# Performance work log

Measured on AMD Instinct MI355X. Metric: run time of the kernel, lower is better.

Reference implementation:

```python
import jax, jax.numpy as jnp
import numpy as np

E, H, F, LE, LD, K, CD, DIN = 256, 8, 1024, 4, 3, 8, 4, 4
B, S = 16, 512
SIG2 = 1.0 ** 2 + 1e-8   # dr_sigma**2 + 1e-8
EPS = 1e-5               # LayerNorm / BatchNorm eps


def _ln(x, w, b):
    m = x.mean(-1, keepdims=True)
    v = ((x - m) ** 2).mean(-1, keepdims=True)
    return (x - m) / jnp.sqrt(v + EPS) * w + b


def _gelu(x):
    return jax.nn.gelu(x, approximate=False)  # torch nn.GELU default = exact erf


def _mha(xq, xkv, qkv_w, qkv_b, out_w, out_b, bias=None):
    # torch nn.MultiheadAttention (batch_first), additive float attn bias broadcast over heads
    wq, wk, wv = jnp.split(qkv_w, 3, axis=0)
    bq, bk, bv = jnp.split(qkv_b, 3)
    q = xq @ wq.T + bq
    k = xkv @ wk.T + bk
    v = xkv @ wv.T + bv
    Bn, Tq, Tk = q.shape[0], q.shape[1], k.shape[1]
    hd = E // H
    qh = q.reshape(Bn, Tq, H, hd)
    kh = k.reshape(Bn, Tk, H, hd)
    vh = v.reshape(Bn, Tk, H, hd)
    s = jnp.einsum('bqhd,bkhd->bhqk', qh, kh) / jnp.sqrt(jnp.asarray(hd, q.dtype))
    if bias is not None:
        s = s + bias[:, None]  # same bias for every head
    p = jax.nn.softmax(s, axis=-1)
    o = jnp.einsum('bhqk,bkhd->bqhd', p, vh).reshape(Bn, Tq, E)
    return o @ out_w.T + out_b


def _forward(x, mask, parent_idx, in_w, in_b, bn_w, bn_b, dr_gamma,
             e_qkv_w, e_qkv_b, e_out_w, e_out_b, e_l1_w, e_l1_b, e_l2_w, e_l2_b,
             e_n1_w, e_n1_b, e_n2_w, e_n2_b,
             parent_w, parent_b, query_embed, c1_w, c1_b, c2_w, c2_b,
             d_sqkv_w, d_sqkv_b, d_sout_w, d_sout_b,
             d_cqkv_w, d_cqkv_b, d_cout_w, d_cout_b,
             d_l1_w, d_l1_b, d_l2_w, d_l2_b,
             d_n1_w, d_n1_b, d_n2_w, d_n2_b, d_n3_w, d_n3_b,
             child_w, child_b, o1_w, o1_b, o2_w, o2_b):
    x = jnp.nan_to_num(x)
    # input_dim==4 convention: (log_pt, dEta, dPhi, log_E)
    coords = jnp.stack([x[..., 1], x[..., 2]], axis=-1)          # [B,S,2]
    # input_proj: Linear -> BatchNorm1d (eval: mean 0, var 1) -> GELU (dropout=identity in eval)
    h = x @ in_w.T + in_b
    h = (h / jnp.sqrt(1.0 + EPS)) * bn_w + bn_b
    h = _gelu(h)
    # dR Gaussian attention bias: [B,S,S]; mask is all-valid so no -inf fill
    d = coords[:, :, None, :] - coords[:, None, :, :]
    dr2 = d[..., 0] ** 2 + d[..., 1] ** 2
    bias = -(dr_gamma[0] * dr2) / (2.0 * SIG2)
    # dR-biased pre-norm encoder
    for i in range(LE):
        hn = _ln(h, e_n1_w[i], e_n1_b[i])
        h = h + _mha(hn, hn, e_qkv_w[i], e_qkv_b[i], e_out_w[i], e_out_b[i], bias)
        hn = _ln(h, e_n2_w[i], e_n2_b[i])
        h = h + _gelu(hn @ e_l1_w[i].T + e_l1_b[i]) @ e_l2_w[i].T + e_l2_b[i]
    memory = jnp.nan_to_num(h)
    parent_logit = (memory @ parent_w.T + parent_b)[..., 0]       # [B,S]
    # conditional decoder queries
    p = memory[jnp.arange(memory.shape[0]), parent_idx]           # [B,E]
    m = mask.astype(memory.dtype)
    g = (memory * m[..., None]).sum(1) / jnp.maximum(m.sum(1, keepdims=True), 1.0)
    cond = _gelu(jnp.concatenate([p, g], -1) @ c1_w.T + c1_b) @ c2_w.T + c2_b
    t = query_embed[None] + cond[:, None]                         # [B,K,E]
    # pre-norm transformer decoder (self-attn, cross-attn, ff)
    for i in range(LD):
        tn = _ln(t, d_n1_w[i], d_n1_b[i])
        t = t + _mha(tn, tn, d_sqkv_w[i], d_sqkv_b[i], d_sout_w[i], d_sout_b[i])
        tn = _ln(t, d_n2_w[i], d_n2_b[i])
        t = t + _mha(tn, memory, d_cqkv_w[i], d_cqkv_b[i], d_cout_w[i], d_cout_b[i])
        tn = _ln(t, d_n3_w[i], d_n3_b[i])
        t = t + _gelu(tn @ d_l1_w[i].T + d_l1_b[i]) @ d_l2_w[i].T + d_l2_b[i]
    child_feat = t @ child_w.T + child_b                          # [B,K,CD]
    obj_logit = (_gelu(t @ o1_w.T + o1_b) @ o2_w.T + o2_b)[..., 0]  # [B,K]
    return parent_logit, child_feat, obj_logit


def setup_inputs() -> dict:
    key = jax.random.key(0)
    ks = iter(jax.random.split(key, 64))
    def w(shape, scale=0.05):
        return jax.random.normal(next(ks), shape, jnp.float32) * scale
    return {
        'x': jax.random.normal(next(ks), (B, S, DIN), jnp.float32),
        'mask': jnp.ones((B, S), dtype=bool),
        'parent_idx': jax.random.randint(next(ks), (B,), 0, S),
        'in_w': w((E, DIN)), 'in_b': jnp.zeros((E,)),
        'bn_w': jnp.ones((E,)), 'bn_b': jnp.zeros((E,)),
        'dr_gamma': jnp.ones((1,)),
        'e_qkv_w': w((LE, 3 * E, E)), 'e_qkv_b': jnp.zeros((LE, 3 * E)),
        'e_out_w': w((LE, E, E)), 'e_out_b': jnp.zeros((LE, E)),
        'e_l1_w': w((LE, F, E)), 'e_l1_b': jnp.zeros((LE, F)),
        'e_l2_w': w((LE, E, F)), 'e_l2_b': jnp.zeros((LE, E)),
        'e_n1_w': jnp.ones((LE, E)), 'e_n1_b': jnp.zeros((LE, E)),
        'e_n2_w': jnp.ones((LE, E)), 'e_n2_b': jnp.zeros((LE, E)),
        'parent_w': w((1, E)), 'parent_b': jnp.zeros((1,)),
        'query_embed': w((K, E), 0.02),
        'c1_w': w((E, 2 * E)), 'c1_b': jnp.zeros((E,)),
        'c2_w': w((E, E)), 'c2_b': jnp.zeros((E,)),
        'd_sqkv_w': w((LD, 3 * E, E)), 'd_sqkv_b': jnp.zeros((LD, 3 * E)),
        'd_sout_w': w((LD, E, E)), 'd_sout_b': jnp.zeros((LD, E)),
        'd_cqkv_w': w((LD, 3 * E, E)), 'd_cqkv_b': jnp.zeros((LD, 3 * E)),
        'd_cout_w': w((LD, E, E)), 'd_cout_b': jnp.zeros((LD, E)),
        'd_l1_w': w((LD, F, E)), 'd_l1_b': jnp.zeros((LD, F)),
        'd_l2_w': w((LD, E, F)), 'd_l2_b': jnp.zeros((LD, E)),
        'd_n1_w': jnp.ones((LD, E)), 'd_n1_b': jnp.zeros((LD, E)),
        'd_n2_w': jnp.ones((LD, E)), 'd_n2_b': jnp.zeros((LD, E)),
        'd_n3_w': jnp.ones((LD, E)), 'd_n3_b': jnp.zeros((LD, E)),
        'child_w': w((CD, E)), 'child_b': jnp.zeros((CD,)),
        'o1_w': w((E, E)), 'o1_b': jnp.zeros((E,)),
        'o2_w': w((1, E)), 'o2_b': jnp.zeros((1,)),
    }


def reference(x, mask, parent_idx, in_w, in_b, bn_w, bn_b, dr_gamma,
              e_qkv_w, e_qkv_b, e_out_w, e_out_b, e_l1_w, e_l1_b, e_l2_w, e_l2_b,
              e_n1_w, e_n1_b, e_n2_w, e_n2_b,
              parent_w, parent_b, query_embed, c1_w, c1_b, c2_w, c2_b,
              d_sqkv_w, d_sqkv_b, d_sout_w, d_sout_b,
              d_cqkv_w, d_cqkv_b, d_cout_w, d_cout_b,
              d_l1_w, d_l1_b, d_l2_w, d_l2_b,
              d_n1_w, d_n1_b, d_n2_w, d_n2_b, d_n3_w, d_n3_b,
              child_w, child_b, o1_w, o1_b, o2_w, o2_b):
    return _forward(x, mask, parent_idx, in_w, in_b, bn_w, bn_b, dr_gamma,
                    e_qkv_w, e_qkv_b, e_out_w, e_out_b, e_l1_w, e_l1_b, e_l2_w, e_l2_b,
                    e_n1_w, e_n1_b, e_n2_w, e_n2_b,
                    parent_w, parent_b, query_embed, c1_w, c1_b, c2_w, c2_b,
                    d_sqkv_w, d_sqkv_b, d_sout_w, d_sout_b,
                    d_cqkv_w, d_cqkv_b, d_cout_w, d_cout_b,
                    d_l1_w, d_l1_b, d_l2_w, d_l2_b,
                    d_n1_w, d_n1_b, d_n2_w, d_n2_b, d_n3_w, d_n3_b,
                    child_w, child_b, o1_w, o1_b, o2_w, o2_b)
```

## Files before the change

kernel.cpp:

```cpp
#include <hip/hip_runtime.h>
#include <math.h>

#define E 256
#define H 8
#define HD 32
#define FF 1024
#define LE 4
#define LDN 3
#define KQ 8
#define CDIM 4
#define DIN 4
#define BATCH 16
#define SEQ 512

typedef __attribute__((ext_vector_type(8))) short s8b;
typedef __attribute__((ext_vector_type(4))) float f32x4;

__device__ __forceinline__ float gelu_f(float x) {
  return 0.5f * x * (1.f + erff(x * 0.70710678118654752f));
}

__device__ __forceinline__ unsigned short f2b(float f) {
  union { float f; unsigned u; } a;
  a.f = f;
  unsigned r = (a.u + 0x7fffu + ((a.u >> 16) & 1u)) >> 16;
  return (unsigned short)r;
}

__device__ __forceinline__ float b2f(unsigned short u) {
  union { unsigned u; float f; } a;
  a.u = ((unsigned)u) << 16;
  return a.f;
}

__device__ __forceinline__ void gload16(const unsigned short* g, unsigned short* l) {
  __builtin_amdgcn_global_load_lds((const __attribute__((address_space(1))) void*)g,
                                   (__attribute__((address_space(3))) void*)l, 16, 0, 0);
}

template <int GELU, int OMODE>
__global__ __launch_bounds__(256) void mfma_gemm64o_kernel(
    const unsigned short* __restrict__ A, const unsigned short* __restrict__ Wt,
    const float* __restrict__ bias, unsigned short* __restrict__ outb,
    unsigned short* __restrict__ vtb, int N, int K) {
  __shared__ __align__(16) unsigned short As[64 * 32];
  __shared__ __align__(16) unsigned short Bs[128 * 32];
  int tid = threadIdx.x;
  int lane = tid & 63, w = tid >> 6;
  int row0 = blockIdx.y * 64, col0 = blockIdx.x * 128;
  int wr = (w >> 1) * 32, wc = (w & 1) * 64;
  f32x4 acc[2][4] = {};

  int sc = lane & 3;
  int srA = w * 16 + (lane >> 2);
  int gcA = (sc ^ ((srA >> 1) & 3)) * 8;
  const unsigned short* ApA = A + (size_t)(row0 + srA) * K + gcA;
  unsigned short* lA = As + (w * 16) * 32;
  int sr0 = w * 32 + (lane >> 2);
  int sr1 = sr0 + 16;
  int gc0 = (sc ^ ((sr0 >> 1) & 3)) * 8;
  int gc1 = (sc ^ ((sr1 >> 1) & 3)) * 8;
  const unsigned short* Bp0 = Wt + (size_t)(col0 + sr0) * K + gc0;
  const unsigned short* Bp1 = Wt + (size_t)(col0 + sr1) * K + gc1;
  unsigned short* lB0 = Bs + (w * 32) * 32;
  unsigned short* lB1 = Bs + (w * 32 + 16) * 32;

  for (int k0 = 0; k0 < K; k0 += 32) {
    __syncthreads();
    gload16(ApA + k0, lA);
    gload16(Bp0 + k0, lB0);
    gload16(Bp1 + k0, lB1);
    __syncthreads();
    int krow = lane & 15, kq = lane >> 4;
    s8b afr[2], bfr[4];
    #pragma unroll
    for (int mi = 0; mi < 2; ++mi) {
      int r = wr + mi * 16 + krow;
      afr[mi] = *(const s8b*)(As + r * 32 + ((kq ^ ((r >> 1) & 3)) * 8));
    }
    #pragma unroll
    for (int ni = 0; ni < 4; ++ni) {
      int r = wc + ni * 16 + krow;
      bfr[ni] = *(const s8b*)(Bs + r * 32 + ((kq ^ ((r >> 1) & 3)) * 8));
    }
    #pragma unroll
    for (int mi = 0; mi < 2; ++mi)
      #pragma unroll
      for (int ni = 0; ni < 4; ++ni)
        acc[mi][ni] = __builtin_amdgcn_mfma_f32_16x16x32_bf16(afr[mi], bfr[ni], acc[mi][ni], 0, 0, 0);
  }

  int cl = lane & 15, rb = (lane >> 4) * 4;
  #pragma unroll
  for (int ni = 0; ni < 4; ++ni) {
    int col = col0 + wc + ni * 16 + cl;
    float bv = bias[col];
    #pragma unroll
    for (int mi = 0; mi < 2; ++mi) {
      #pragma unroll
      for (int j = 0; j < 4; ++j) {
        int row = row0 + wr + mi * 16 + rb + j;
        float v = acc[mi][ni][j] + bv;
        if (GELU) v = gelu_f(v);
        if (OMODE == 1) {
          outb[(size_t)row * N + col] = f2b(v);
        } else {
          int b = row >> 9, s = row & 511;
          int sect = col >> 8, hh = (col >> 5) & 7, d = col & 31;
          if (sect < 2)
            outb[((((size_t)sect * BATCH + b) * H + hh) * SEQ + s) * HD + d] = f2b(v);
          else
            vtb[(((size_t)b * H + hh) * HD + d) * SEQ + s] = f2b(v);
        }
      }
    }
  }
}

__global__ __launch_bounds__(256) void mfma_gemm32_kernel(
    const unsigned short* __restrict__ A, const unsigned short* __restrict__ Wt,
    const float* __restrict__ bias, const float* __restrict__ resid,
    float* __restrict__ outf, int M, int N, int K) {
  __shared__ __align__(16) unsigned short As[32 * 32];
  __shared__ __align__(16) unsigned short Bs[128 * 32];
  int tid = threadIdx.x;
  int lane = tid & 63, w = tid >> 6;
  int row0 = blockIdx.y * 32, col0 = blockIdx.x * 128;
  int wr = (w & 1) * 16, wc = (w >> 1) * 64;
  f32x4 acc[4] = {};

  int sc = lane & 3;
  int srA = w * 16 + (lane >> 2);
  int gcA = (sc ^ ((srA >> 1) & 3)) * 8;
  const unsigned short* ApA = A + (size_t)(row0 + (srA & 31)) * K + gcA;
  unsigned short* lA = As + ((w & 1) * 16) * 32;
  int sr0 = w * 32 + (lane >> 2);
  int sr1 = sr0 + 16;
  int gc0 = (sc ^ ((sr0 >> 1) & 3)) * 8;
  int gc1 = (sc ^ ((sr1 >> 1) & 3)) * 8;
  const unsigned short* Bp0 = Wt + (size_t)(col0 + sr0) * K + gc0;
  const unsigned short* Bp1 = Wt + (size_t)(col0 + sr1) * K + gc1;
  unsigned short* lB0 = Bs + (w * 32) * 32;
  unsigned short* lB1 = Bs + (w * 32 + 16) * 32;

  for (int k0 = 0; k0 < K; k0 += 32) {
    __syncthreads();
    if (w < 2) gload16(ApA + k0, lA);
    gload16(Bp0 + k0, lB0);
    gload16(Bp1 + k0, lB1);
    __syncthreads();
    int krow = lane & 15, kq = lane >> 4;
    int ra = wr + krow;
    s8b afr = *(const s8b*)(As + ra * 32 + ((kq ^ ((ra >> 1) & 3)) * 8));
    #pragma unroll
    for (int ni = 0; ni < 4; ++ni) {
      int r = wc + ni * 16 + krow;
      s8b bfr = *(const s8b*)(Bs + r * 32 + ((kq ^ ((r >> 1) & 3)) * 8));
      acc[ni] = __builtin_amdgcn_mfma_f32_16x16x32_bf16(afr, bfr, acc[ni], 0, 0, 0);
    }
  }

  int cl = lane & 15, rb = (lane >> 4) * 4;
  #pragma unroll
  for (int ni = 0; ni < 4; ++ni) {
    int col = col0 + wc + ni * 16 + cl;
    float bv = bias[col];
    #pragma unroll
    for (int j = 0; j < 4; ++j) {
      int row = row0 + wr + rb + j;
      outf[(size_t)row * N + col] = acc[ni][j] + bv + resid[(size_t)row * N + col];
    }
  }
}

__global__ __launch_bounds__(256) void mfma_attn_kernel(
    const unsigned short* __restrict__ qkb, const unsigned short* __restrict__ vt,
    const float2* __restrict__ carr, const float* __restrict__ gamma_p,
    unsigned short* __restrict__ out) {
  __shared__ __align__(16) unsigned short P[4][16 * 64];
  int tid = threadIdx.x, lane = tid & 63, w = tid >> 6;
  int qt = blockIdx.x, h = blockIdx.y, b = blockIdx.z;
  int q0 = qt * 64 + w * 16;
  const unsigned short* qh = qkb + (((size_t)b * H + h) * SEQ) * HD;
  const unsigned short* kh = qkb + ((((size_t)BATCH + b) * H + h) * SEQ) * HD;
  const unsigned short* vh = vt + (((size_t)b * H + h) * HD) * SEQ;
  int r16 = lane & 15, q4 = lane >> 4;
  s8b qa = *(const s8b*)(qh + (size_t)(q0 + r16) * HD + q4 * 8);
  float eq[4], pq[4];
  #pragma unroll
  for (int j = 0; j < 4; ++j) {
    float2 c = carr[b * SEQ + q0 + q4 * 4 + j];
    eq[j] = c.x; pq[j] = c.y;
  }
  float gam = gamma_p[0] * 0.49999999500000004f;
  const float scale = 0.17677669529663687f;
  float m[4], lsum[4];
  #pragma unroll
  for (int j = 0; j < 4; ++j) { m[j] = -1e30f; lsum[j] = 0.f; }
  f32x4 o0 = {}, o1 = {};
  const f32x4 zf = {0.f, 0.f, 0.f, 0.f};
  unsigned short* pw = &P[w][0];

  for (int t = 0; t < SEQ / 64; ++t) {
    int k0 = t * 64;
    f32x4 sf[4];
    #pragma unroll
    for (int f = 0; f < 4; ++f) {
      s8b bk = *(const s8b*)(kh + (size_t)(k0 + f * 16 + r16) * HD + q4 * 8);
      sf[f] = __builtin_amdgcn_mfma_f32_16x16x32_bf16(qa, bk, zf, 0, 0, 0);
    }
    float ek[4], pk[4];
    #pragma unroll
    for (int f = 0; f < 4; ++f) {
      float2 c = carr[b * SEQ + k0 + f * 16 + r16];
      ek[f] = c.x; pk[f] = c.y;
    }
    float sc_[4][4];
    float tmax[4] = {-1e30f, -1e30f, -1e30f, -1e30f};
    #pragma unroll
    for (int f = 0; f < 4; ++f)
      #pragma unroll
      for (int j = 0; j < 4; ++j) {
        float de = eq[j] - ek[f], dp = pq[j] - pk[f];
        float v = sf[f][j] * scale - gam * (de * de + dp * dp);
        sc_[f][j] = v;
        tmax[j] = fmaxf(tmax[j], v);
      }
    #pragma unroll
    for (int j = 0; j < 4; ++j) {
      #pragma unroll
      for (int off = 1; off < 16; off <<= 1)
        tmax[j] = fmaxf(tmax[j], __shfl_xor(tmax[j], off));
      float mn = fmaxf(m[j], tmax[j]);
      float al = __expf(m[j] - mn);
      m[j] = mn;
      lsum[j] *= al;
      o0[j] *= al;
      o1[j] *= al;
    }
    __syncthreads();
    #pragma unroll
    for (int f = 0; f < 4; ++f)
      #pragma unroll
      for (int j = 0; j < 4; ++j) {
        float p = __expf(sc_[f][j] - m[j]);
        lsum[j] += p;
        int prow = q4 * 4 + j;
        int c = f * 16 + r16;
        int chunk = (c >> 3) ^ (prow & 7);
        pw[prow * 64 + chunk * 8 + (c & 7)] = f2b(p);
      }
    __syncthreads();
    #pragma unroll
    for (int ks = 0; ks < 2; ++ks) {
      int chunk = (ks * 4 + q4) ^ (r16 & 7);
      s8b pa = *(const s8b*)(pw + r16 * 64 + chunk * 8);
      s8b v0 = *(const s8b*)(vh + (size_t)r16 * SEQ + k0 + ks * 32 + q4 * 8);
      s8b v1 = *(const s8b*)(vh + (size_t)(16 + r16) * SEQ + k0 + ks * 32 + q4 * 8);
      o0 = __builtin_amdgcn_mfma_f32_16x16x32_bf16(pa, v0, o0, 0, 0, 0);
      o1 = __builtin_amdgcn_mfma_f32_16x16x32_bf16(pa, v1, o1, 0, 0, 0);
    }
  }
  #pragma unroll
  for (int j = 0; j < 4; ++j) {
    #pragma unroll
    for (int off = 1; off < 16; off <<= 1)
      lsum[j] += __shfl_xor(lsum[j], off);
    float inv = 1.f / lsum[j];
    size_t rbase = ((size_t)(b * SEQ + q0 + q4 * 4 + j)) * E + h * HD;
    out[rbase + r16] = f2b(o0[j] * inv);
    out[rbase + 16 + r16] = f2b(o1[j] * inv);
  }
}

__global__ void coords_kernel(const float* __restrict__ x, float2* __restrict__ carr) {
  int i = blockIdx.x * 256 + threadIdx.x;
  if (i >= BATCH * SEQ) return;
  carr[i] = make_float2(x[(size_t)i * DIN + 1], x[(size_t)i * DIN + 2]);
}

__global__ void f2b_kernel(const float* __restrict__ in, unsigned short* __restrict__ out, int n4) {
  int i = blockIdx.x * 256 + threadIdx.x;
  if (i >= n4) return;
  float4 v = ((const float4*)in)[i];
  ushort4 o;
  o.x = f2b(v.x); o.y = f2b(v.y); o.z = f2b(v.z); o.w = f2b(v.w);
  ((ushort4*)out)[i] = o;
}

__global__ void cvt_all_kernel(const float* __restrict__ w0, const float* __restrict__ w1,
                               const float* __restrict__ w2, const float* __restrict__ w3,
                               unsigned short* __restrict__ o0, unsigned short* __restrict__ o1,
                               unsigned short* __restrict__ o2, unsigned short* __restrict__ o3) {
  const int n0 = LE * 3 * E * E / 4, n1 = LE * E * E / 4;
  const int n2 = LE * FF * E / 4, n3 = LE * E * FF / 4;
  int j = blockIdx.x * 256 + threadIdx.x;
  const float* src; unsigned short* dst;
  if (j < n0) { src = w0; dst = o0; }
  else if ((j -= n0) < n1) { src = w1; dst = o1; }
  else if ((j -= n1) < n2) { src = w2; dst = o2; }
  else if ((j -= n2) < n3) { src = w3; dst = o3; }
  else return;
  float4 v = ((const float4*)src)[j];
  ushort4 o;
  o.x = f2b(v.x); o.y = f2b(v.y); o.z = f2b(v.z); o.w = f2b(v.w);
  ((ushort4*)dst)[j] = o;
}

__global__ void kvw_remap_kernel(const float* __restrict__ w, const float* __restrict__ b,
                                 unsigned short* __restrict__ wout, float* __restrict__ bout) {
  int i = blockIdx.x * 256 + threadIdx.x;
  if (i < 1536) bout[i] = b[(i >> 9) * 768 + 256 + (i & 511)];
  if (i >= 98304) return;
  int row = i >> 6, cc = i & 63;
  int l = row >> 9, rr = row & 511;
  const float* src = w + ((size_t)l * 768 + 256 + rr) * 256 + cc * 4;
  float4 v = *(const float4*)src;
  ushort4 o;
  o.x = f2b(v.x); o.y = f2b(v.y); o.z = f2b(v.z); o.w = f2b(v.w);
  *(ushort4*)(wout + (size_t)row * 256 + cc * 4) = o;
}

__global__ __launch_bounds__(256) void input_proj_ln_kernel(
    const float* __restrict__ x, const float* __restrict__ in_w, const float* __restrict__ in_b,
    const float* __restrict__ bn_w, const float* __restrict__ bn_b,
    const float* __restrict__ nw, const float* __restrict__ nb,
    float* __restrict__ h, unsigned short* __restrict__ hn) {
  __shared__ float sred[4];
  __shared__ float vred[4];
  int row = blockIdx.x, e = threadIdx.x;
  const float* xr = x + (size_t)row * DIN;
  float v = in_b[e];
  #pragma unroll
  for (int i = 0; i < DIN; ++i) v += xr[i] * in_w[e * DIN + i];
  v = v * (1.0f / sqrtf(1.0f + 1e-5f)) * bn_w[e] + bn_b[e];
  v = gelu_f(v);
  h[(size_t)row * 256 + e] = v;
  int lane = e & 63, w = e >> 6;
  float s = v;
  #pragma unroll
  for (int off = 32; off > 0; off >>= 1) s += __shfl_xor(s, off);
  if (lane == 0) sred[w] = s;
  __syncthreads();
  float mean = (sred[0] + sred[1] + sred[2] + sred[3]) * (1.f / 256);
  float d = v - mean;
  float vr = d * d;
  #pragma unroll
  for (int off = 32; off > 0; off >>= 1) vr += __shfl_xor(vr, off);
  if (lane == 0) vred[w] = vr;
  __syncthreads();
  float inv = rsqrtf((vred[0] + vred[1] + vred[2] + vred[3]) * (1.f / 256) + 1e-5f);
  hn[(size_t)row * 256 + e] = f2b(d * inv * nw[e] + nb[e]);
}

__global__ __launch_bounds__(256) void ln_bf16_kernel(
    const float* __restrict__ in, const float* __restrict__ w,
    const float* __restrict__ b, unsigned short* __restrict__ out) {
  int r = blockIdx.x * 4 + (threadIdx.x >> 6);
  int l = threadIdx.x & 63;
  const float* p = in + (size_t)r * E;
  float v0 = p[l], v1 = p[l + 64], v2 = p[l + 128], v3 = p[l + 192];
  float s = v0 + v1 + v2 + v3;
  for (int off = 32; off > 0; off >>= 1) s += __shfl_xor(s, off);
  float mean = s * (1.f / E);
  float d0 = v0 - mean, d1 = v1 - mean, d2 = v2 - mean, d3 = v3 - mean;
  float var = d0 * d0 + d1 * d1 + d2 * d2 + d3 * d3;
  for (int off = 32; off > 0; off >>= 1) var += __shfl_xor(var, off);
  float inv = rsqrtf(var * (1.f / E) + 1e-5f);
  unsigned short* o = out + (size_t)r * E;
  o[l]       = f2b(d0 * inv * w[l]       + b[l]);
  o[l + 64]  = f2b(d1 * inv * w[l + 64]  + b[l + 64]);
  o[l + 128] = f2b(d2 * inv * w[l + 128] + b[l + 128]);
  o[l + 192] = f2b(d3 * inv * w[l + 192] + b[l + 192]);
}


template <int N, int GELU>
__global__ __launch_bounds__(256) void dec_ln_gemv_kernel(
    const float* __restrict__ t, const float* __restrict__ nw, const float* __restrict__ nb,
    const float* __restrict__ W, const float* __restrict__ bias, float* __restrict__ outg) {
  __shared__ float X[8][256];
  __shared__ float Pp[4][64][9];
  int b = blockIdx.x, by = blockIdx.y, tid = threadIdx.x;
  const float* tg = t + (size_t)b * 2048;
  int w = tid >> 6, l = tid & 63;
  #pragma unroll
  for (int rr = 0; rr < 2; ++rr) {
    int r = w * 2 + rr;
    float v0 = tg[r * 256 + l], v1 = tg[r * 256 + 64 + l];
    float v2 = tg[r * 256 + 128 + l], v3 = tg[r * 256 + 192 + l];
    float s = v0 + v1 + v2 + v3;
    for (int o = 32; o > 0; o >>= 1) s += __shfl_xor(s, o);
    float mean = s * (1.f / 256);
    float d0 = v0 - mean, d1 = v1 - mean, d2 = v2 - mean, d3 = v3 - mean;
    float var = d0 * d0 + d1 * d1 + d2 * d2 + d3 * d3;
    for (int o = 32; o > 0; o >>= 1) var += __shfl_xor(var, o);
    float inv = rsqrtf(var * (1.f / 256) + 1e-5f);
    X[r][l] = d0 * inv * nw[l] + nb[l];
    X[r][l + 64] = d1 * inv * nw[l + 64] + nb[l + 64];
    X[r][l + 128] = d2 * inv * nw[l + 128] + nb[l + 128];
    X[r][l + 192] = d3 * inv * nw[l + 192] + nb[l + 192];
  }
  __syncthreads();
  int j = tid & 63, kq = tid >> 6;
  int col = by * 64 + j;
  const float4* wp = (const float4*)(W + (size_t)col * 256 + kq * 64);
  float acc[8] = {};
  #pragma unroll
  for (int kk = 0; kk < 16; ++kk) {
    float4 wv = wp[kk];
    int base = kq * 64 + kk * 4;
    #pragma unroll
    for (int r = 0; r < 8; ++r) {
      float4 xv = *(const float4*)&X[r][base];
      acc[r] += xv.x * wv.x + xv.y * wv.y + xv.z * wv.z + xv.w * wv.w;
    }
  }
  #pragma unroll
  for (int r = 0; r < 8; ++r) Pp[kq][j][r] = acc[r];
  __syncthreads();
  for (int i = tid; i < 512; i += 256) {
    int r = i & 7, j2 = i >> 3;
    float v = Pp[0][j2][r] + Pp[1][j2][r] + Pp[2][j2][r] + Pp[3][j2][r] + bias[by * 64 + j2];
    if (GELU) v = gelu_f(v);
    outg[((size_t)b * 8 + r) * N + by * 64 + j2] = v;
  }
}

__global__ __launch_bounds__(256) void dec_selfattn_sout_kernel(
    const float* __restrict__ qkvg, const float* __restrict__ W, const float* __restrict__ bias,
    float* __restrict__ t) {
  __shared__ float QK[8][768];
  __shared__ float S[512];
  __shared__ float X[8][256];
  __shared__ float Pp[4][64][9];
  int b = blockIdx.x, by = blockIdx.y, tid = threadIdx.x;
  const float* qg = qkvg + (size_t)b * 8 * 768;
  for (int i = tid; i < 6144; i += 256) ((float*)QK)[i] = qg[i];
  __syncthreads();
  for (int t2 = tid; t2 < 512; t2 += 256) {
    int h = t2 >> 6, q = (t2 >> 3) & 7, k = t2 & 7;
    const float* qp = &QK[q][h * 32];
    const float* kp = &QK[k][256 + h * 32];
    float d = 0.f;
    #pragma unroll
    for (int jj = 0; jj < 32; ++jj) d += qp[jj] * kp[jj];
    S[t2] = d * 0.17677669529663687f;
  }
  __syncthreads();
  if (tid < 64) {
    float* row = &S[tid * 8];
    float m = row[0];
    #pragma unroll
    for (int k = 1; k < 8; ++k) m = fmaxf(m, row[k]);
    float sum = 0.f;
    #pragma unroll
    for (int k = 0; k < 8; ++k) { float e = __expf(row[k] - m); row[k] = e; sum += e; }
    float inv = 1.f / sum;
    #pragma unroll
    for (int k = 0; k < 8; ++k) row[k] *= inv;
  }
  __syncthreads();
  for (int i = tid; i < 2048; i += 256) {
    int q = i >> 8, c = i & 255, h = c >> 5;
    const float* pr = &S[h * 64 + q * 8];
    float acc = 0.f;
    #pragma unroll
    for (int k = 0; k < 8; ++k) acc += pr[k] * QK[k][512 + c];
    X[q][c] = acc;
  }
  __syncthreads();
  int j = tid & 63, kq = tid >> 6;
  int col = by * 64 + j;
  const float4* wp = (const float4*)(W + (size_t)col * 256 + kq * 64);
  float acc[8] = {};
  #pragma unroll
  for (int kk = 0; kk < 16; ++kk) {
    float4 wv = wp[kk];
    int base = kq * 64 + kk * 4;
    #pragma unroll
    for (int r = 0; r < 8; ++r) {
      float4 xv = *(const float4*)&X[r][base];
      acc[r] += xv.x * wv.x + xv.y * wv.y + xv.z * wv.z + xv.w * wv.w;
    }
  }
  #pragma unroll
  for (int r = 0; r < 8; ++r) Pp[kq][j][r] = acc[r];
  __syncthreads();
  for (int i = tid; i < 512; i += 256) {
    int r = i & 7, j2 = i >> 3;
    float v = Pp[0][j2][r] + Pp[1][j2][r] + Pp[2][j2][r] + Pp[3][j2][r] + bias[by * 64 + j2];
    t[((size_t)b * 8 + r) * 256 + by * 64 + j2] += v;
  }
}

__global__ __launch_bounds__(256) void dec_gemv_resid_kernel(
    const float* __restrict__ Xg, const float* __restrict__ W, const float* __restrict__ bias,
    float* __restrict__ t) {
  __shared__ float X[8][256];
  __shared__ float Pp[4][64][9];
  int b = blockIdx.x, by = blockIdx.y, tid = threadIdx.x;
  const float* xg = Xg + (size_t)b * 2048;
  for (int i = tid; i < 2048; i += 256) ((float*)X)[i] = xg[i];
  __syncthreads();
  int j = tid & 63, kq = tid >> 6;
  int col = by * 64 + j;
  const float4* wp = (const float4*)(W + (size_t)col * 256 + kq * 64);
  float acc[8] = {};
  #pragma unroll
  for (int kk = 0; kk < 16; ++kk) {
    float4 wv = wp[kk];
    int base = kq * 64 + kk * 4;
    #pragma unroll
    for (int r = 0; r < 8; ++r) {
      float4 xv = *(const float4*)&X[r][base];
      acc[r] += xv.x * wv.x + xv.y * wv.y + xv.z * wv.z + xv.w * wv.w;
    }
  }
  #pragma unroll
  for (int r = 0; r < 8; ++r) Pp[kq][j][r] = acc[r];
  __syncthreads();
  for (int i = tid; i < 512; i += 256) {
    int r = i & 7, j2 = i >> 3;
    float v = Pp[0][j2][r] + Pp[1][j2][r] + Pp[2][j2][r] + Pp[3][j2][r] + bias[by * 64 + j2];
    t[((size_t)b * 8 + r) * 256 + by * 64 + j2] += v;
  }
}

__global__ __launch_bounds__(256) void dec_ffn2_kernel(
    const float* __restrict__ MIDg, const float* __restrict__ W, const float* __restrict__ bias,
    float* __restrict__ t) {
  __shared__ float X[8][1024];
  __shared__ float Pp[4][64][9];
  int b = blockIdx.x, by = blockIdx.y, tid = threadIdx.x;
  const float* xg = MIDg + (size_t)b * 8192;
  for (int i = tid; i < 8192; i += 256) ((float*)X)[i] = xg[i];
  __syncthreads();
  int j = tid & 63, kq = tid >> 6;
  int col = by * 64 + j;
  const float4* wp = (const float4*)(W + (size_t)col * 1024 + kq * 256);
  float acc[8] = {};
  #pragma unroll 8
  for (int kk = 0; kk < 64; ++kk) {
    float4 wv = wp[kk];
    int base = kq * 256 + kk * 4;
    #pragma unroll
    for (int r = 0; r < 8; ++r) {
      float4 xv = *(const float4*)&X[r][base];
      acc[r] += xv.x * wv.x + xv.y * wv.y + xv.z * wv.z + xv.w * wv.w;
    }
  }
  #pragma unroll
  for (int r = 0; r < 8; ++r) Pp[kq][j][r] = acc[r];
  __syncthreads();
  for (int i = tid; i < 512; i += 256) {
    int r = i & 7, j2 = i >> 3;
    float v = Pp[0][j2][r] + Pp[1][j2][r] + Pp[2][j2][r] + Pp[3][j2][r] + bias[by * 64 + j2];
    t[((size_t)b * 8 + r) * 256 + by * 64 + j2] += v;
  }
}

__global__ __launch_bounds__(256) void cross_attn_ln_kernel(
    const float* __restrict__ t, const float* __restrict__ nw, const float* __restrict__ nb,
    const float* __restrict__ cqw, const float* __restrict__ cqb,
    const unsigned short* __restrict__ KV, int koff, int voff, float* __restrict__ out) {
  __shared__ float X[256];
  __shared__ float sv[512];
  __shared__ float red[256];
  __shared__ float qv[32];
  __shared__ float pvred[8][32];
  __shared__ float sred[4], vred[4];
  int tid = threadIdx.x;
  int bid = blockIdx.x;
  int q = bid % KQ;
  int h = (bid / KQ) % H;
  int b = bid / (KQ * H);
  {
    float v = t[((size_t)(b * KQ + q)) * 256 + tid];
    int lane = tid & 63, w = tid >> 6;
    float s = v;
    #pragma unroll
    for (int off = 32; off > 0; off >>= 1) s += __shfl_xor(s, off);
    if (lane == 0) sred[w] = s;
    __syncthreads();
    float mean = (sred[0] + sred[1] + sred[2] + sred[3]) * (1.f / 256);
    float d = v - mean;
    float vr = d * d;
    #pragma unroll
    for (int off = 32; off > 0; off >>= 1) vr += __shfl_xor(vr, off);
    if (lane == 0) vred[w] = vr;
    __syncthreads();
    float inv = rsqrtf((vred[0] + vred[1] + vred[2] + vred[3]) * (1.f / 256) + 1e-5f);
    X[tid] = d * inv * nw[tid] + nb[tid];
  }
  __syncthreads();
  {
    int dd = tid >> 3, part = tid & 7;
    int col = h * HD + dd;
    const float4* wp = (const float4*)(cqw + (size_t)col * 256 + part * 32);
    float acc = 0.f;
    #pragma unroll
    for (int kk = 0; kk < 8; ++kk) {
      float4 wv = wp[kk];
      float4 xv = *(const float4*)&X[part * 32 + kk * 4];
      acc += xv.x * wv.x + xv.y * wv.y + xv.z * wv.z + xv.w * wv.w;
    }
    red[tid] = acc;
  }
  __syncthreads();
  if (tid < 32) {
    float acc = 0.f;
    #pragma unroll
    for (int p = 0; p < 8; ++p) acc += red[tid * 8 + p];
    qv[tid] = acc + cqb[h * HD + tid];
  }
  __syncthreads();
  const float scale = 0.17677669529663687f;
  for (int k = tid; k < SEQ; k += 256) {
    const unsigned short* kp = KV + ((size_t)(b * SEQ + k)) * 1536 + koff + h * HD;
    float d = 0.f;
    #pragma unroll
    for (int j4 = 0; j4 < 4; ++j4) {
      s8b kv8 = *(const s8b*)(kp + j4 * 8);
      #pragma unroll
      for (int j = 0; j < 8; ++j)
        d += qv[j4 * 8 + j] * b2f((unsigned short)kv8[j]);
    }
    sv[k] = d * scale;
  }
  __syncthreads();
  float m = -1e30f;
  for (int k = tid; k < SEQ; k += 256) m = fmaxf(m, sv[k]);
  red[tid] = m; __syncthreads();
  for (int s = 128; s > 0; s >>= 1) {
    if (tid < s) red[tid] = fmaxf(red[tid], red[tid + s]);
    __syncthreads();
  }
  m = red[0]; __syncthreads();
  float lsum = 0.f;
  for (int k = tid; k < SEQ; k += 256) { float e = __expf(sv[k] - m); sv[k] = e; lsum += e; }
  red[tid] = lsum; __syncthreads();
  for (int s = 128; s > 0; s >>= 1) {
    if (tid < s) red[tid] += red[tid + s];
    __syncthreads();
  }
  float denom = red[0];
  int d = tid & 31, g = tid >> 5;
  float acc = 0.f;
  for (int k = g; k < SEQ; k += 8)
    acc += sv[k] * b2f(KV[((size_t)(b * SEQ + k)) * 1536 + voff + h * HD + d]);
  pvred[g][d] = acc;
  __syncthreads();
  if (tid < 32) {
    float r = 0.f;
    #pragma unroll
    for (int gg = 0; gg < 8; ++gg) r += pvred[gg][tid];
    out[((size_t)(b * KQ + q)) * E + h * HD + tid] = r / denom;
  }
}

__global__ __launch_bounds__(256) void pool_gather_kernel(
    const float* __restrict__ mem, const int* __restrict__ pidx, float* __restrict__ pg) {
  __shared__ float red[8][32];
  int b = blockIdx.x, cy = blockIdx.y, tid = threadIdx.x;
  int c = cy * 32 + (tid & 31), g = tid >> 5;
  float s = 0.f;
  for (int r = g; r < SEQ; r += 8)
    s += mem[((size_t)b * SEQ + r) * E + c];
  red[g][tid & 31] = s;
  __syncthreads();
  if (tid < 32) {
    float t = 0.f;
    #pragma unroll
    for (int g2 = 0; g2 < 8; ++g2) t += red[g2][tid];
    pg[(size_t)b * 512 + 256 + cy * 32 + tid] = t * (1.f / SEQ);
    pg[(size_t)b * 512 + cy * 32 + tid] = mem[((size_t)b * SEQ + pidx[b]) * E + cy * 32 + tid];
  }
}

__global__ void cond_kernel(const float* __restrict__ pg, const float* __restrict__ c1w,
                            const float* __restrict__ c1b, const float* __restrict__ c2w,
                            const float* __restrict__ c2b, const float* __restrict__ qe,
                            float* __restrict__ t) {
  __shared__ float PG[512];
  __shared__ float C1[256];
  int b = blockIdx.x, c = threadIdx.x;
  PG[c] = pg[(size_t)b * 512 + c];
  PG[c + 256] = pg[(size_t)b * 512 + 256 + c];
  __syncthreads();
  const float4* wp = (const float4*)(c1w + (size_t)c * 512);
  float acc = c1b[c];
  #pragma unroll 8
  for (int kk = 0; kk < 128; ++kk) {
    float4 wv = wp[kk];
    int base = kk * 4;
    acc += PG[base] * wv.x + PG[base + 1] * wv.y + PG[base + 2] * wv.z + PG[base + 3] * wv.w;
  }
  C1[c] = gelu_f(acc);
  __syncthreads();
  const float4* wp2 = (const float4*)(c2w + (size_t)c * 256);
  float acc2 = c2b[c];
  #pragma unroll 8
  for (int kk = 0; kk < 64; ++kk) {
    float4 wv = wp2[kk];
    int base = kk * 4;
    acc2 += C1[base] * wv.x + C1[base + 1] * wv.y + C1[base + 2] * wv.z + C1[base + 3] * wv.w;
  }
  #pragma unroll
  for (int k = 0; k < KQ; ++k)
    t[((size_t)b * KQ + k) * E + c] = qe[k * E + c] + acc2;
}

__global__ void head_kernel(const float* __restrict__ t,
                            const float* __restrict__ childw, const float* __restrict__ childb,
                            const float* __restrict__ o1w, const float* __restrict__ o1b,
                            const float* __restrict__ o2w, const float* __restrict__ o2b,
                            float* __restrict__ out_child, float* __restrict__ out_obj) {
  __shared__ float tr[256];
  __shared__ float red[256];
  int r = blockIdx.x, c = threadIdx.x;
  tr[c] = t[(size_t)r * E + c];
  __syncthreads();
  const float4* wp = (const float4*)(o1w + (size_t)c * 256);
  float acc = o1b[c];
  #pragma unroll 8
  for (int kk = 0; kk < 64; ++kk) {
    float4 wv = wp[kk];
    int base = kk * 4;
    acc += tr[base] * wv.x + tr[base + 1] * wv.y + tr[base + 2] * wv.z + tr[base + 3] * wv.w;
  }
  red[c] = gelu_f(acc) * o2w[c];
  __syncthreads();
  for (int s = 128; s > 0; s >>= 1) {
    if (c < s) red[c] += red[c + s];
    __syncthreads();
  }
  if (c == 0) out_obj[r] = red[0] + o2b[0];
  __syncthreads();
  #pragma unroll
  for (int j = 0; j < CDIM; ++j) {
    red[c] = tr[c] * childw[j * E + c];
    __syncthreads();
    for (int s = 128; s > 0; s >>= 1) {
      if (c < s) red[c] += red[c + s];
      __syncthreads();
    }
    if (c == 0) out_child[r * CDIM + j] = red[0] + childb[j];
    __syncthreads();
  }
}

__global__ void rowdot_kernel(const float* __restrict__ A, const float* __restrict__ w,
                              const float* __restrict__ bias, float* __restrict__ out) {
  int r = blockIdx.x, l = threadIdx.x;
  const float* p = A + (size_t)r * E;
  float s = p[l] * w[l] + p[l + 64] * w[l + 64] + p[l + 128] * w[l + 128] + p[l + 192] * w[l + 192];
  for (int off = 32; off > 0; off >>= 1) s += __shfl_xor(s, off);
  if (l == 0) out[r] = s + bias[0];
}

extern "C" void kernel_launch(void* const* d_in, const int* in_sizes, int n_in,
                              void* d_out, int out_size, void* d_ws, size_t ws_size,
                              hipStream_t stream) {
  const float* x          = (const float*)d_in[0];
  const int*   parent_idx = (const int*)d_in[2];
  const float* in_w  = (const float*)d_in[3];
  const float* in_b  = (const float*)d_in[4];
  const float* bn_w  = (const float*)d_in[5];
  const float* bn_b  = (const float*)d_in[6];
  const float* dr_gamma = (const float*)d_in[7];
  const float* e_qkv_w = (const float*)d_in[8];
  const float* e_qkv_b = (const float*)d_in[9];
  const float* e_out_w = (const float*)d_in[10];
  const float* e_out_b = (const float*)d_in[11];
  const float* e_l1_w = (const float*)d_in[12];
  const float* e_l1_b = (const float*)d_in[13];
  const float* e_l2_w = (const float*)d_in[14];
  const float* e_l2_b = (const float*)d_in[15];
  const float* e_n1_w = (const float*)d_in[16];
  const float* e_n1_b = (const float*)d_in[17];
  const float* e_n2_w = (const float*)d_in[18];
  const float* e_n2_b = (const float*)d_in[19];
  const float* parent_w = (const float*)d_in[20];
  const float* parent_b = (const float*)d_in[21];
  const float* query_embed = (const float*)d_in[22];
  const float* c1_w = (const float*)d_in[23];
  const float* c1_b = (const float*)d_in[24];
  const float* c2_w = (const float*)d_in[25];
  const float* c2_b = (const float*)d_in[26];
  const float* d_sqkv_w = (const float*)d_in[27];
  const float* d_sqkv_b = (const float*)d_in[28];
  const float* d_sout_w = (const float*)d_in[29];
  const float* d_sout_b = (const float*)d_in[30];
  const float* d_cqkv_w = (const float*)d_in[31];
  const float* d_cqkv_b = (const float*)d_in[32];
  const float* d_cout_w = (const float*)d_in[33];
  const float* d_cout_b = (const float*)d_in[34];
  const float* d_l1_w = (const float*)d_in[35];
  const float* d_l1_b = (const float*)d_in[36];
  const float* d_l2_w = (const float*)d_in[37];
  const float* d_l2_b = (const float*)d_in[38];
  const float* d_n1_w = (const float*)d_in[39];
  const float* d_n1_b = (const float*)d_in[40];
  const float* d_n2_w = (const float*)d_in[41];
  const float* d_n2_b = (const float*)d_in[42];
  const float* d_n3_w = (const float*)d_in[43];
  const float* d_n3_b = (const float*)d_in[44];
  const float* child_w = (const float*)d_in[45];
  const float* child_b = (const float*)d_in[46];
  const float* o1_w = (const float*)d_in[47];
  const float* o1_b = (const float*)d_in[48];
  const float* o2_w = (const float*)d_in[49];
  const float* o2_b = (const float*)d_in[50];

  float* out = (float*)d_out;
  const int ROWS = BATCH * SEQ;
  const int TROWS = BATCH * KQ;

  float* ws = (float*)d_ws;
  float* h         = ws;
  float* attnout_d = h + (size_t)ROWS * E;
  float* pg        = attnout_d + (size_t)TROWS * E;
  float* tbuf      = pg + BATCH * 2 * E;
  float* qkv_t     = tbuf + (size_t)TROWS * E;
  float* dmid      = qkv_t + (size_t)TROWS * 3 * E;
  float* kvb3      = dmid + (size_t)TROWS * FF;
  unsigned short* kv_bf   = (unsigned short*)(kvb3 + 1536);
  unsigned short* hn_bf   = kv_bf + (size_t)ROWS * 1536;
  unsigned short* attn_bf = hn_bf + (size_t)ROWS * E;
  unsigned short* mid_bf  = attn_bf + (size_t)ROWS * E;
  unsigned short* eqkv_bf = mid_bf + (size_t)ROWS * FF;
  unsigned short* eout_bf = eqkv_bf + (size_t)LE * 3 * E * E;
  unsigned short* el1_bf  = eout_bf + (size_t)LE * E * E;
  unsigned short* el2_bf  = el1_bf + (size_t)LE * FF * E;
  unsigned short* kvw_bf  = el2_bf + (size_t)LE * E * FF;
  float2* carr = (float2*)(kvw_bf + (size_t)1536 * 256);
  unsigned short* qkb = mid_bf;
  unsigned short* vtb = mid_bf + (size_t)2 * ROWS * E;

  {
    const int total_quads = (LE * 3 * E * E + LE * E * E + LE * FF * E + LE * E * FF) / 4;
    cvt_all_kernel<<<(total_quads + 255) / 256, 256, 0, stream>>>(
        e_qkv_w, e_out_w, e_l1_w, e_l2_w, eqkv_bf, eout_bf, el1_bf, el2_bf);
  }
  kvw_remap_kernel<<<384, 256, 0, stream>>>(d_cqkv_w, d_cqkv_b, kvw_bf, kvb3);
  coords_kernel<<<(BATCH * SEQ + 255) / 256, 256, 0, stream>>>(x, carr);

  input_proj_ln_kernel<<<ROWS, 256, 0, stream>>>(x, in_w, in_b, bn_w, bn_b,
                                                 e_n1_w, e_n1_b, h, hn_bf);

  for (int i = 0; i < LE; ++i) {
    const float* qb = e_qkv_b + (size_t)i * 3 * E;
    const float* ob = e_out_b + (size_t)i * E;
    const float* l1b = e_l1_b + (size_t)i * FF;
    const float* l2b = e_l2_b + (size_t)i * E;
    if (i > 0)
      ln_bf16_kernel<<<ROWS / 4, 256, 0, stream>>>(h, e_n1_w + i * E, e_n1_b + i * E, hn_bf);
    mfma_gemm64o_kernel<0, 2><<<dim3(6, 128), 256, 0, stream>>>(
        hn_bf, eqkv_bf + (size_t)i * 3 * E * E, qb, qkb, vtb, 3 * E, E);
    mfma_attn_kernel<<<dim3(SEQ / 64, H, BATCH), 256, 0, stream>>>(qkb, vtb, carr, dr_gamma, attn_bf);
    mfma_gemm32_kernel<<<dim3(2, 256), 256, 0, stream>>>(
        attn_bf, eout_bf + (size_t)i * E * E, ob, h, h, ROWS, E, E);
    ln_bf16_kernel<<<ROWS / 4, 256, 0, stream>>>(h, e_n2_w + i * E, e_n2_b + i * E, hn_bf);
    mfma_gemm64o_kernel<1, 1><<<dim3(8, 128), 256, 0, stream>>>(
        hn_bf, el1_bf + (size_t)i * FF * E, l1b, mid_bf, nullptr, FF, E);
    mfma_gemm32_kernel<<<dim3(2, 256), 256, 0, stream>>>(
        mid_bf, el2_bf + (size_t)i * E * FF, l2b, h, h, ROWS, E, FF);
  }

  rowdot_kernel<<<ROWS, 64, 0, stream>>>(h, parent_w, parent_b, out);

  pool_gather_kernel<<<dim3(BATCH, 8), 256, 0, stream>>>(h, parent_idx, pg);
  cond_kernel<<<BATCH, 256, 0, stream>>>(pg, c1_w, c1_b, c2_w, c2_b, query_embed, tbuf);

  f2b_kernel<<<(ROWS * E / 4 + 255) / 256, 256, 0, stream>>>(h, hn_bf, ROWS * E / 4);
  mfma_gemm64o_kernel<0, 1><<<dim3(12, 128), 256, 0, stream>>>(
      hn_bf, kvw_bf, kvb3, kv_bf, nullptr, 3 * E * 2, E);

  for (int i = 0; i < LDN; ++i) {
    dec_ln_gemv_kernel<768, 0><<<dim3(BATCH, 12), 256, 0, stream>>>(
        tbuf, d_n1_w + i * E, d_n1_b + i * E,
        d_sqkv_w + (size_t)i * 3 * E * E, d_sqkv_b + (size_t)i * 3 * E, qkv_t);
    dec_selfattn_sout_kernel<<<dim3(BATCH, 4), 256, 0, stream>>>(
        qkv_t, d_sout_w + (size_t)i * E * E, d_sout_b + (size_t)i * E, tbuf);
    cross_attn_ln_kernel<<<BATCH * H * KQ, 256, 0, stream>>>(
        tbuf, d_n2_w + i * E, d_n2_b + i * E,
        d_cqkv_w + (size_t)i * 3 * E * E, d_cqkv_b + (size_t)i * 3 * E,
        kv_bf, i * 512, i * 512 + 256, attnout_d);
    dec_gemv_resid_kernel<<<dim3(BATCH, 4), 256, 0, stream>>>(
        attnout_d, d_cout_w + (size_t)i * E * E, d_cout_b + (size_t)i * E, tbuf);
    dec_ln_gemv_kernel<1024, 1><<<dim3(BATCH, 16), 256, 0, stream>>>(
        tbuf, d_n3_w + i * E, d_n3_b + i * E,
        d_l1_w + (size_t)i * FF * E, d_l1_b + (size_t)i * FF, dmid);
    dec_ffn2_kernel<<<dim3(BATCH, 4), 256, 0, stream>>>(
        dmid, d_l2_w + (size_t)i * E * FF, d_l2_b + (size_t)i * E, tbuf);
  }

  head_kernel<<<TROWS, 256, 0, stream>>>(tbuf, child_w, child_b, o1_w, o1_b, o2_w, o2_b,
                                         out + ROWS, out + ROWS + TROWS * CDIM);
}
```

Baseline: 748.6 us.

## Fuse LayerNorm and bf16 cast into residual GEMM epilogue with full-row tiles

The residual-add GEMM now gives each block 32 full rows of all 256 output columns, so the epilogue can compute the row LayerNorm across the block and write the bf16 normalized activations directly. This removes the separate ln_bf16 kernels and the final f2b cast kernel. Each layer saves launches and a full read of the fp32 hidden state. In exchange there are half as many blocks (256 instead of 512) and more accumulator registers per thread, which may lower occupancy for the K=1024 GEMM.

```diff
diff --git a/kernel.cpp b/kernel.cpp
--- a/kernel.cpp
+++ b/kernel.cpp
@@ -117,58 +117,115 @@
   }
 }
 
-__global__ __launch_bounds__(256) void mfma_gemm32_kernel(
+template <int LNMODE>
+__global__ __launch_bounds__(256) void mfma_gemm32n256_ln_kernel(
     const unsigned short* __restrict__ A, const unsigned short* __restrict__ Wt,
-    const float* __restrict__ bias, const float* __restrict__ resid,
-    float* __restrict__ outf, int M, int N, int K) {
+    const float* __restrict__ bias, float* __restrict__ h,
+    const float* __restrict__ nw, const float* __restrict__ nb,
+    unsigned short* __restrict__ hn, int K) {
   __shared__ __align__(16) unsigned short As[32 * 32];
-  __shared__ __align__(16) unsigned short Bs[128 * 32];
+  __shared__ __align__(16) unsigned short Bs[256 * 32];
+  __shared__ float psum[2][32];
+  __shared__ float pvar[2][32];
   int tid = threadIdx.x;
   int lane = tid & 63, w = tid >> 6;
-  int row0 = blockIdx.y * 32, col0 = blockIdx.x * 128;
-  int wr = (w & 1) * 16, wc = (w >> 1) * 64;
-  f32x4 acc[4] = {};
+  int row0 = blockIdx.x * 32;
+  int wr = (w & 1) * 16, wc = (w >> 1) * 128;
+  int ch = w >> 1;
+  f32x4 acc[8] = {};
 
   int sc = lane & 3;
   int srA = w * 16 + (lane >> 2);
   int gcA = (sc ^ ((srA >> 1) & 3)) * 8;
   const unsigned short* ApA = A + (size_t)(row0 + (srA & 31)) * K + gcA;
   unsigned short* lA = As + ((w & 1) * 16) * 32;
-  int sr0 = w * 32 + (lane >> 2);
-  int sr1 = sr0 + 16;
-  int gc0 = (sc ^ ((sr0 >> 1) & 3)) * 8;
-  int gc1 = (sc ^ ((sr1 >> 1) & 3)) * 8;
-  const unsigned short* Bp0 = Wt + (size_t)(col0 + sr0) * K + gc0;
-  const unsigned short* Bp1 = Wt + (size_t)(col0 + sr1) * K + gc1;
-  unsigned short* lB0 = Bs + (w * 32) * 32;
-  unsigned short* lB1 = Bs + (w * 32 + 16) * 32;
+  const unsigned short* BpB[4];
+  unsigned short* lB[4];
+  #pragma unroll
+  for (int is = 0; is < 4; ++is) {
+    int srB = w * 64 + is * 16 + (lane >> 2);
+    int gcB = (sc ^ ((srB >> 1) & 3)) * 8;
+    BpB[is] = Wt + (size_t)srB * K + gcB;
+    lB[is] = Bs + (w * 64 + is * 16) * 32;
+  }
 
   for (int k0 = 0; k0 < K; k0 += 32) {
     __syncthreads();
     if (w < 2) gload16(ApA + k0, lA);
-    gload16(Bp0 + k0, lB0);
-    gload16(Bp1 + k0, lB1);
+    #pragma unroll
+    for (int is = 0; is < 4; ++is) gload16(BpB[is] + k0, lB[is]);
     __syncthreads();
     int krow = lane & 15, kq = lane >> 4;
     int ra = wr + krow;
     s8b afr = *(const s8b*)(As + ra * 32 + ((kq ^ ((ra >> 1) & 3)) * 8));
     #pragma unroll
-    for (int ni = 0; ni < 4; ++ni) {
-      int r = wc + ni * 16 + krow;
+    for (int nf = 0; nf < 8; ++nf) {
+      int r = wc + nf * 16 + krow;
       s8b bfr = *(const s8b*)(Bs + r * 32 + ((kq ^ ((r >> 1) & 3)) * 8));
-      acc[ni] = __builtin_amdgcn_mfma_f32_16x16x32_bf16(afr, bfr, acc[ni], 0, 0, 0);
+      acc[nf] = __builtin_amdgcn_mfma_f32_16x16x32_bf16(afr, bfr, acc[nf], 0, 0, 0);
     }
   }
 
   int cl = lane & 15, rb = (lane >> 4) * 4;
   #pragma unroll
-  for (int ni = 0; ni < 4; ++ni) {
-    int col = col0 + wc + ni * 16 + cl;
+  for (int nf = 0; nf < 8; ++nf) {
+    int col = wc + nf * 16 + cl;
     float bv = bias[col];
     #pragma unroll
     for (int j = 0; j < 4; ++j) {
       int row = row0 + wr + rb + j;
-      outf[(size_t)row * N + col] = acc[ni][j] + bv + resid[(size_t)row * N + col];
+      float v = acc[nf][j] + bv + h[(size_t)row * 256 + col];
+      acc[nf][j] = v;
+      h[(size_t)row * 256 + col] = v;
+    }
+  }
+  if (LNMODE == 0) {
+    float mean_[4], inv_[4];
+    #pragma unroll
+    for (int j = 0; j < 4; ++j) {
+      float s = 0.f;
+      #pragma unroll
+      for (int nf = 0; nf < 8; ++nf) s += acc[nf][j];
+      s += __shfl_xor(s, 1); s += __shfl_xor(s, 2);
+      s += __shfl_xor(s, 4); s += __shfl_xor(s, 8);
+      if (cl == 0) psum[ch][wr + rb + j] = s;
+    }
+    __syncthreads();
+    #pragma unroll
+    for (int j = 0; j < 4; ++j)
+      mean_[j] = (psum[0][wr + rb + j] + psum[1][wr + rb + j]) * (1.f / 256);
+    #pragma unroll
+    for (int j = 0; j < 4; ++j) {
+      float vv = 0.f;
+      #pragma unroll
+      for (int nf = 0; nf < 8; ++nf) { float d = acc[nf][j] - mean_[j]; vv += d * d; }
+      vv += __shfl_xor(vv, 1); vv += __shfl_xor(vv, 2);
+      vv += __shfl_xor(vv, 4); vv += __shfl_xor(vv, 8);
+      if (cl == 0) pvar[ch][wr + rb + j] = vv;
+    }
+    __syncthreads();
+    #pragma unroll
+    for (int j = 0; j < 4; ++j)
+      inv_[j] = rsqrtf((pvar[0][wr + rb + j] + pvar[1][wr + rb + j]) * (1.f / 256) + 1e-5f);
+    #pragma unroll
+    for (int nf = 0; nf < 8; ++nf) {
+      int col = wc + nf * 16 + cl;
+      float nwv = nw[col], nbv = nb[col];
+      #pragma unroll
+      for (int j = 0; j < 4; ++j) {
+        int row = row0 + wr + rb + j;
+        hn[(size_t)row * 256 + col] = f2b((acc[nf][j] - mean_[j]) * inv_[j] * nwv + nbv);
+      }
+    }
+  } else {
+    #pragma unroll
+    for (int nf = 0; nf < 8; ++nf) {
+      int col = wc + nf * 16 + cl;
+      #pragma unroll
+      for (int j = 0; j < 4; ++j) {
+        int row = row0 + wr + rb + j;
+        hn[(size_t)row * 256 + col] = f2b(acc[nf][j]);
+      }
     }
   }
 }
@@ -277,15 +334,6 @@
   int i = blockIdx.x * 256 + threadIdx.x;
   if (i >= BATCH * SEQ) return;
   carr[i] = make_float2(x[(size_t)i * DIN + 1], x[(size_t)i * DIN + 2]);
-}
-
-__global__ void f2b_kernel(const float* __restrict__ in, unsigned short* __restrict__ out, int n4) {
-  int i = blockIdx.x * 256 + threadIdx.x;
-  if (i >= n4) return;
-  float4 v = ((const float4*)in)[i];
-  ushort4 o;
-  o.x = f2b(v.x); o.y = f2b(v.y); o.z = f2b(v.z); o.w = f2b(v.w);
-  ((ushort4*)out)[i] = o;
 }
 
 __global__ void cvt_all_kernel(const float* __restrict__ w0, const float* __restrict__ w1,
@@ -351,27 +399,6 @@
   __syncthreads();
   float inv = rsqrtf((vred[0] + vred[1] + vred[2] + vred[3]) * (1.f / 256) + 1e-5f);
   hn[(size_t)row * 256 + e] = f2b(d * inv * nw[e] + nb[e]);
-}
-
-__global__ __launch_bounds__(256) void ln_bf16_kernel(
-    const float* __restrict__ in, const float* __restrict__ w,
-    const float* __restrict__ b, unsigned short* __restrict__ out) {
-  int r = blockIdx.x * 4 + (threadIdx.x >> 6);
-  int l = threadIdx.x & 63;
-  const float* p = in + (size_t)r * E;
-  float v0 = p[l], v1 = p[l + 64], v2 = p[l + 128], v3 = p[l + 192];
-  float s = v0 + v1 + v2 + v3;
-  for (int off = 32; off > 0; off >>= 1) s += __shfl_xor(s, off);
-  float mean = s * (1.f / E);
-  float d0 = v0 - mean, d1 = v1 - mean, d2 = v2 - mean, d3 = v3 - mean;
-  float var = d0 * d0 + d1 * d1 + d2 * d2 + d3 * d3;
-  for (int off = 32; off > 0; off >>= 1) var += __shfl_xor(var, off);
-  float inv = rsqrtf(var * (1.f / E) + 1e-5f);
-  unsigned short* o = out + (size_t)r * E;
-  o[l]       = f2b(d0 * inv * w[l]       + b[l]);
-  o[l + 64]  = f2b(d1 * inv * w[l + 64]  + b[l + 64]);
-  o[l + 128] = f2b(d2 * inv * w[l + 128] + b[l + 128]);
-  o[l + 192] = f2b(d3 * inv * w[l + 192] + b[l + 192]);
 }
 
 
@@ -854,18 +881,22 @@
     const float* ob = e_out_b + (size_t)i * E;
     const float* l1b = e_l1_b + (size_t)i * FF;
     const float* l2b = e_l2_b + (size_t)i * E;
-    if (i > 0)
-      ln_bf16_kernel<<<ROWS / 4, 256, 0, stream>>>(h, e_n1_w + i * E, e_n1_b + i * E, hn_bf);
     mfma_gemm64o_kernel<0, 2><<<dim3(6, 128), 256, 0, stream>>>(
         hn_bf, eqkv_bf + (size_t)i * 3 * E * E, qb, qkb, vtb, 3 * E, E);
     mfma_attn_kernel<<<dim3(SEQ / 64, H, BATCH), 256, 0, stream>>>(qkb, vtb, carr, dr_gamma, attn_bf);
-    mfma_gemm32_kernel<<<dim3(2, 256), 256, 0, stream>>>(
-        attn_bf, eout_bf + (size_t)i * E * E, ob, h, h, ROWS, E, E);
-    ln_bf16_kernel<<<ROWS / 4, 256, 0, stream>>>(h, e_n2_w + i * E, e_n2_b + i * E, hn_bf);
+    mfma_gemm32n256_ln_kernel<0><<<256, 256, 0, stream>>>(
+        attn_bf, eout_bf + (size_t)i * E * E, ob, h,
+        e_n2_w + i * E, e_n2_b + i * E, hn_bf, E);
     mfma_gemm64o_kernel<1, 1><<<dim3(8, 128), 256, 0, stream>>>(
         hn_bf, el1_bf + (size_t)i * FF * E, l1b, mid_bf, nullptr, FF, E);
-    mfma_gemm32_kernel<<<dim3(2, 256), 256, 0, stream>>>(
-        mid_bf, el2_bf + (size_t)i * E * FF, l2b, h, h, ROWS, E, FF);
+    if (i < LE - 1)
+      mfma_gemm32n256_ln_kernel<0><<<256, 256, 0, stream>>>(
+          mid_bf, el2_bf + (size_t)i * E * FF, l2b, h,
+          e_n1_w + (i + 1) * E, e_n1_b + (i + 1) * E, hn_bf, FF);
+    else
+      mfma_gemm32n256_ln_kernel<1><<<256, 256, 0, stream>>>(
+          mid_bf, el2_bf + (size_t)i * E * FF, l2b, h,
+          nullptr, nullptr, hn_bf, FF);
   }
 
   rowdot_kernel<<<ROWS, 64, 0, stream>>>(h, parent_w, parent_b, out);
@@ -873,7 +904,6 @@
   pool_gather_kernel<<<dim3(BATCH, 8), 256, 0, stream>>>(h, parent_idx, pg);
   cond_kernel<<<BATCH, 256, 0, stream>>>(pg, c1_w, c1_b, c2_w, c2_b, query_embed, tbuf);
 
-  f2b_kernel<<<(ROWS * E / 4 + 255) / 256, 256, 0, stream>>>(h, hn_bf, ROWS * E / 4);
   mfma_gemm64o_kernel<0, 1><<<dim3(12, 128), 256, 0, stream>>>(
       hn_bf, kvw_bf, kvb3, kv_bf, nullptr, 3 * E * 2, E);
 
```

Result: slower. 766.0 us (+2.3%).
